# Optimization experiments

Measured on AMD Instinct MI355X. Metric: run time of the kernel, lower is better.

The kernel has to match this reference:

```python
import jax, jax.numpy as jnp
import numpy as np

EPS = 1e-5
TOPK = 2
SHARED_RATIO = 0.1

B, S, H = 2, 1024, 2048
NH, DH, R = 16, 128, 64
CQ, CKV = 1024, 512
E, I, NS = 8, 1024, 2


def rmsnorm(x, w):
    return x * jax.lax.rsqrt(jnp.mean(x * x, axis=-1, keepdims=True) + EPS) * w


def rope_cos_sin(seq_len, dim):
    inv = 1.0 / (10000.0 ** (jnp.arange(0, dim, 2, dtype=jnp.float32) / dim))
    t = jnp.arange(seq_len, dtype=jnp.float32)[:, None] * inv[None, :]  # [S, dim/2]
    return jnp.cos(t), jnp.sin(t)


def apply_rope(x, cos, sin):
    # rotate-half on last dim; cos/sin broadcast over leading dims
    x1, x2 = jnp.split(x, 2, axis=-1)
    return jnp.concatenate([x1 * cos - x2 * sin, x2 * cos + x1 * sin], axis=-1)


def swiglu(x, w1, w3, w2):
    return (jax.nn.silu(x @ w1) * (x @ w3)) @ w2


def setup_inputs() -> dict:
    key = jax.random.key(0)
    ks = jax.random.split(key, 24)
    sc = 0.02
    d = {
        'x': jax.random.normal(ks[0], (B, S, H), jnp.float32),
        'attn_norm_w': jnp.ones((H,), jnp.float32),
        'ffn_norm_w': jnp.ones((H,), jnp.float32),
        'W_dq': sc * jax.random.normal(ks[1], (H, CQ), jnp.float32),
        'q_norm_w': jnp.ones((CQ,), jnp.float32),
        'W_uq': sc * jax.random.normal(ks[2], (CQ, NH * DH), jnp.float32),
        'W_qr': sc * jax.random.normal(ks[3], (CQ, NH * R), jnp.float32),
        'W_dkv': sc * jax.random.normal(ks[4], (H, CKV), jnp.float32),
        'kv_norm_w': jnp.ones((CKV,), jnp.float32),
        'W_uk': sc * jax.random.normal(ks[5], (CKV, NH * DH), jnp.float32),
        'W_uv': sc * jax.random.normal(ks[6], (CKV, NH * DH), jnp.float32),
        'W_kr': sc * jax.random.normal(ks[7], (H, R), jnp.float32),
        'W_o': sc * jax.random.normal(ks[8], (NH * DH, H), jnp.float32),
        'centroids': sc * jax.random.normal(ks[9], (E, H), jnp.float32),
        'expert_bias': jnp.zeros((E,), jnp.float32),
        'w1': sc * jax.random.normal(ks[10], (E, H, I), jnp.float32),
        'w3': sc * jax.random.normal(ks[11], (E, H, I), jnp.float32),
        'w2': sc * jax.random.normal(ks[12], (E, I, H), jnp.float32),
        'w1s': sc * jax.random.normal(ks[13], (NS, H, I), jnp.float32),
        'w3s': sc * jax.random.normal(ks[14], (NS, H, I), jnp.float32),
        'w2s': sc * jax.random.normal(ks[15], (NS, I, H), jnp.float32),
    }
    return d


def reference(x, attn_norm_w, ffn_norm_w, W_dq, q_norm_w, W_uq, W_qr, W_dkv,
              kv_norm_w, W_uk, W_uv, W_kr, W_o, centroids, expert_bias,
              w1, w3, w2, w1s, w3s, w2s):
    b, s, h = x.shape
    r = W_kr.shape[1]
    nh = W_qr.shape[1] // r
    dh = W_uq.shape[1] // nh

    # ---- MLA attention (pre-norm) ----
    hn = rmsnorm(x, attn_norm_w)
    cq = rmsnorm(hn @ W_dq, q_norm_w)                    # [b,s,CQ] compressed query latent
    q = (cq @ W_uq).reshape(b, s, nh, dh)                # content queries
    qr = (cq @ W_qr).reshape(b, s, nh, r)                # rope queries
    ckv = rmsnorm(hn @ W_dkv, kv_norm_w)                 # [b,s,CKV] compressed kv latent
    k = (ckv @ W_uk).reshape(b, s, nh, dh)
    v = (ckv @ W_uv).reshape(b, s, nh, dh)
    kr = hn @ W_kr                                       # [b,s,r] shared rope key

    cos, sin = rope_cos_sin(s, r)
    qr = apply_rope(qr, cos[None, :, None, :], sin[None, :, None, :])
    kr = apply_rope(kr, cos[None, :, :], sin[None, :, :])

    scale = 1.0 / np.sqrt(dh + r).astype(np.float32)
    scores = (jnp.einsum('bqhd,bkhd->bhqk', q, k)
              + jnp.einsum('bqhr,bkr->bhqk', qr, kr)) * scale
    causal = jnp.tril(jnp.ones((s, s), dtype=bool))
    scores = jnp.where(causal[None, None], scores, jnp.finfo(scores.dtype).min)
    attn = jax.nn.softmax(scores, axis=-1)
    attn_out = jnp.einsum('bhqk,bkhd->bqhd', attn, v).reshape(b, s, nh * dh) @ W_o
    x = x + attn_out

    # ---- aux-loss-free MoE (pre-norm) ----
    h2 = rmsnorm(x, ffn_norm_w).reshape(b * s, h)
    gate_scores = jax.nn.sigmoid(h2 @ centroids.T)       # [T,E]
    _, idx = jax.lax.top_k(gate_scores + expert_bias[None, :], TOPK)  # bias only for selection
    gw = jnp.take_along_axis(gate_scores, idx, axis=1)
    gw = gw / jnp.sum(gw, axis=1, keepdims=True)
    dense_w = jnp.sum(jax.nn.one_hot(idx, gate_scores.shape[1], dtype=h2.dtype) * gw[..., None], axis=1)  # [T,E]

    moe = jnp.zeros_like(h2)
    for e in range(w1.shape[0]):
        moe = moe + dense_w[:, e:e + 1] * swiglu(h2, w1[e], w3[e], w2[e])
    for si in range(w1s.shape[0]):
        moe = moe + SHARED_RATIO * swiglu(h2, w1s[si], w3s[si], w2s[si])

    return x + moe.reshape(b, s, h)
```

## Files before the change

### kernel.cpp

```cpp
#include <hip/hip_runtime.h>
#include <hip/hip_bf16.h>
#include <math.h>

typedef unsigned short u16;
typedef __attribute__((ext_vector_type(8))) short s8v;
typedef __attribute__((ext_vector_type(4))) short s4v;
typedef __attribute__((ext_vector_type(4))) float f4v;

#define B_   2
#define S_   1024
#define T_   2048
#define H_   2048
#define NH_  16
#define DH_  128
#define R_   64
#define CQ_  1024
#define CKV_ 512
#define DQK_ 192
#define E_   8
#define I_   1024
#define NS_  2

__device__ __forceinline__ float us2f(u16 u){
  unsigned int i = ((unsigned int)u) << 16; float f; __builtin_memcpy(&f, &i, 4); return f;
}
__device__ __forceinline__ u16 f2us(float f){
  unsigned int i; __builtin_memcpy(&i, &f, 4);
  unsigned int r = i + 0x7fffu + ((i >> 16) & 1u);
  return (u16)(r >> 16);
}
__device__ __forceinline__ f4v MFMA_B16(s8v a, s8v b, f4v c){
  return __builtin_amdgcn_mfma_f32_16x16x32_bf16(a, b, c, 0, 0, 0);
}

typedef const __attribute__((address_space(1))) void* gas_ptr;
typedef __attribute__((address_space(3))) void* las_ptr;
__device__ __forceinline__ void gload16(const void* g, void* l){
  __builtin_amdgcn_global_load_lds((gas_ptr)g, (las_ptr)l, 16, 0, 0);
}

__global__ void rope_table_kernel(float* __restrict__ cosT, float* __restrict__ sinT){
  int i = blockIdx.x * 256 + threadIdx.x;
  if (i >= S_ * 32) return;
  int s = i >> 5, f = i & 31;
  double inv = exp(-(double)f / 32.0 * log(10000.0));
  double t = (double)s * inv;
  cosT[i] = (float)cos(t);
  sinT[i] = (float)sin(t);
}

__global__ __launch_bounds__(256) void ttc_kernel(const float* __restrict__ in, u16* __restrict__ outp,
                                                  int Kd, int Nd, size_t zs, int rowoff){
  __shared__ float tile[64][65];
  size_t ibase = (size_t)blockIdx.z * Kd * Nd;
  size_t obase = (size_t)blockIdx.z * zs;
  int k0 = blockIdx.y * 64, n0 = blockIdx.x * 64;
  int tid = threadIdx.x;
  int tx = tid & 15, ty = tid >> 4;
  #pragma unroll
  for (int pp = 0; pp < 4; pp++){
    int kk = pp * 16 + ty;
    f4v v = *(const f4v*)(in + ibase + (size_t)(k0 + kk) * Nd + n0 + tx * 4);
    tile[kk][tx * 4 + 0] = v[0];
    tile[kk][tx * 4 + 1] = v[1];
    tile[kk][tx * 4 + 2] = v[2];
    tile[kk][tx * 4 + 3] = v[3];
  }
  __syncthreads();
  #pragma unroll
  for (int pp = 0; pp < 4; pp++){
    int nn = pp * 16 + ty;
    s4v o;
    #pragma unroll
    for (int j = 0; j < 4; j++) o[j] = (short)f2us(tile[tx * 4 + j][nn]);
    *(s4v*)(outp + obase + (size_t)(rowoff + n0 + nn) * Kd + k0 + tx * 4) = o;
  }
}

__global__ __launch_bounds__(256) void rmsnorm_kernel(const float* __restrict__ in, const float* __restrict__ w,
                                                      u16* __restrict__ outb, float* __restrict__ outf, int D){
  int t = blockIdx.x;
  const float* row = in + (size_t)t * D;
  float ss = 0.f;
  for (int i = threadIdx.x * 4; i < D; i += 1024){
    f4v v = *(const f4v*)(row + i);
    ss += v[0]*v[0] + v[1]*v[1] + v[2]*v[2] + v[3]*v[3];
  }
  #pragma unroll
  for (int m = 1; m < 64; m <<= 1) ss += __shfl_xor(ss, m);
  __shared__ float red[4];
  if ((threadIdx.x & 63) == 0) red[threadIdx.x >> 6] = ss;
  __syncthreads();
  float tot = red[0] + red[1] + red[2] + red[3];
  float r = 1.0f / sqrtf(tot / (float)D + 1e-5f);
  for (int i = threadIdx.x * 4; i < D; i += 1024){
    f4v v = *(const f4v*)(row + i);
    f4v wv = *(const f4v*)(w + i);
    s4v ob;
    f4v of;
    #pragma unroll
    for (int j = 0; j < 4; j++){ of[j] = v[j] * r * wv[j]; ob[j] = (short)f2us(of[j]); }
    *(s4v*)(outb + (size_t)t * D + i) = ob;
    if (outf) *(f4v*)(outf + (size_t)t * D + i) = of;
  }
}

template<int OUTMODE, bool AGATHER>
__device__ __forceinline__ void gemm_core(const u16* __restrict__ A, int lda,
                                          const u16* __restrict__ Bt, int K, int M,
                                          const int* __restrict__ arows,
                                          float* __restrict__ outf0, float* __restrict__ outf1,
                                          float* __restrict__ outf2,
                                          u16* __restrict__ outb0, u16* __restrict__ outb1,
                                          int ldc0, int ldc1, int split, int split2,
                                          const float* __restrict__ resid,
                                          int bm0, int bn0){
  __shared__ u16 As[2][128 * 32];
  __shared__ u16 Bs[2][128 * 32];
  int tid = threadIdx.x;
  int w = tid >> 6, lane = tid & 63;
  int wr = w >> 2, wc = w & 3;
  int g = lane >> 4, l16 = lane & 15;

  f4v acc[4][2];
  #pragma unroll
  for (int m = 0; m < 4; m++)
    #pragma unroll
    for (int n = 0; n < 2; n++) acc[m][n] = (f4v)0.0f;

  int c = tid;
  int row = c >> 2;
  int sc = (c & 3) ^ ((c >> 3) & 3);
  int grow = bm0 + row;
  int ar;
  if (AGATHER) ar = arows[(grow < M) ? grow : 0];
  else         ar = (grow < M) ? grow : 0;
  const u16* asrc = A + (size_t)ar * lda + sc * 8;
  const u16* bsrc = Bt + (size_t)(bn0 + row) * K + sc * 8;
  int dst = (w * 64) * 8;
  int apos = (g ^ ((l16 >> 1) & 3)) * 8;

  int nt = K >> 5;
  gload16(asrc, &As[0][dst]);
  gload16(bsrc, &Bs[0][dst]);

  int cur = 0;
  for (int t = 0; t < nt; ++t){
    if (t + 1 < nt){
      int kn = (t + 1) * 32;
      gload16(asrc + kn, &As[cur ^ 1][dst]);
      gload16(bsrc + kn, &Bs[cur ^ 1][dst]);
      asm volatile("s_waitcnt vmcnt(2)" ::: "memory");
    } else {
      asm volatile("s_waitcnt vmcnt(0)" ::: "memory");
    }
    __builtin_amdgcn_s_barrier();
    asm volatile("" ::: "memory");
    s8v af[4], bf[2];
    #pragma unroll
    for (int m = 0; m < 4; m++) af[m] = *(const s8v*)(&As[cur][(wr * 64 + m * 16 + l16) * 32 + apos]);
    #pragma unroll
    for (int n = 0; n < 2; n++) bf[n] = *(const s8v*)(&Bs[cur][(wc * 32 + n * 16 + l16) * 32 + apos]);
    __builtin_amdgcn_s_setprio(1);
    #pragma unroll
    for (int m = 0; m < 4; m++)
      #pragma unroll
      for (int n = 0; n < 2; n++)
        acc[m][n] = MFMA_B16(af[m], bf[n], acc[m][n]);
    __builtin_amdgcn_s_setprio(0);
    asm volatile("" ::: "memory");
    __builtin_amdgcn_s_barrier();
    cur ^= 1;
  }

  #pragma unroll
  for (int m = 0; m < 4; m++)
    #pragma unroll
    for (int n = 0; n < 2; n++){
      int ccol = bn0 + wc * 32 + n * 16 + l16;
      #pragma unroll
      for (int j = 0; j < 4; j++){
        int r = wr * 64 + m * 16 + g * 4 + j;
        int gr = bm0 + r;
        if (gr >= M) continue;
        float v = acc[m][n][j];
        if (OUTMODE == 0){
          outf0[(size_t)gr * ldc0 + ccol] = v;
        } else if (OUTMODE == 1){
          outb0[(size_t)gr * ldc0 + ccol] = f2us(v);
        } else if (OUTMODE == 2){
          outf0[(size_t)gr * ldc0 + ccol] = v + resid[(size_t)gr * ldc0 + ccol];
        } else if (OUTMODE == 4){
          if (ccol < split) outb0[(size_t)gr * ldc0 + ccol] = f2us(v);
          else              outb1[(size_t)gr * ldc1 + (ccol - split)] = f2us(v);
        } else {
          if (ccol < split)       outf0[(size_t)gr * ldc0 + ccol] = v;
          else if (ccol < split2) outf1[(size_t)gr * ldc1 + (ccol - split)] = v;
          else if (ccol < split2 + 64) outf2[(size_t)gr * 64 + (ccol - split2)] = v;
        }
      }
    }
}

template<int OUTMODE>
__global__ __launch_bounds__(512) void gemm_kernel(const u16* __restrict__ A, int lda,
                                                   const u16* __restrict__ Bt, int K, int M,
                                                   float* __restrict__ outf0, float* __restrict__ outf1,
                                                   float* __restrict__ outf2,
                                                   u16* __restrict__ outb0, u16* __restrict__ outb1,
                                                   int ldc0, int ldc1, int split, int split2,
                                                   const float* __restrict__ resid){
  int gx = gridDim.x;
  int nwg = gx * gridDim.y;
  int orig = blockIdx.y * gx + blockIdx.x;
  int wg = orig;
  if ((nwg & 7) == 0) wg = (orig & 7) * (nwg >> 3) + (orig >> 3);
  int bx = wg % gx, by = wg / gx;
  gemm_core<OUTMODE, false>(A, lda, Bt, K, M, nullptr,
                            outf0, outf1, outf2, outb0, outb1, ldc0, ldc1, split, split2, resid,
                            by * 128, bx * 128);
}

__global__ __launch_bounds__(256) void build_qcat_kernel(const u16* __restrict__ qbuf, const u16* __restrict__ qrb,
                                                         const float* __restrict__ cosT, const float* __restrict__ sinT,
                                                         u16* __restrict__ qcat){
  size_t i8 = ((size_t)blockIdx.x * 256 + threadIdx.x) * 8;
  const size_t total = (size_t)B_ * NH_ * S_ * DQK_;
  if (i8 >= total) return;
  int d = (int)(i8 % DQK_); size_t rem = i8 / DQK_;
  int s = (int)(rem % S_); rem /= S_;
  int h = (int)(rem % NH_); int b = (int)(rem / NH_);
  int t = b * S_ + s;
  s8v o;
  if (d < DH_){
    o = *(const s8v*)(qbuf + (size_t)t * H_ + h * DH_ + d);
  } else {
    int r0 = d - DH_;
    int rr0 = r0 & 31;
    const u16* qp = qrb + (size_t)t * (NH_ * R_) + h * R_;
    #pragma unroll
    for (int j = 0; j < 8; j++){
      float c = cosT[s * 32 + rr0 + j], sn = sinT[s * 32 + rr0 + j];
      float lo = us2f(qp[rr0 + j]), hi = us2f(qp[rr0 + 32 + j]);
      float val = (r0 < 32) ? (lo * c - hi * sn) : (hi * c + lo * sn);
      o[j] = (short)f2us(val);
    }
  }
  *(s8v*)(qcat + i8) = o;
}

__global__ __launch_bounds__(256) void build_kcat_kernel(const u16* __restrict__ kbuf, const float* __restrict__ krb,
                                                         const float* __restrict__ cosT, const float* __restrict__ sinT,
                                                         u16* __restrict__ kcat){
  size_t i8 = ((size_t)blockIdx.x * 256 + threadIdx.x) * 8;
  const size_t total = (size_t)B_ * NH_ * S_ * DQK_;
  if (i8 >= total) return;
  int d = (int)(i8 % DQK_); size_t rem = i8 / DQK_;
  int s = (int)(rem % S_); rem /= S_;
  int h = (int)(rem % NH_); int b = (int)(rem / NH_);
  int t = b * S_ + s;
  s8v o;
  if (d < DH_){
    o = *(const s8v*)(kbuf + (size_t)t * H_ + h * DH_ + d);
  } else {
    int r0 = d - DH_;
    int rr0 = r0 & 31;
    const float* kp = krb + (size_t)t * R_;
    #pragma unroll
    for (int j = 0; j < 8; j++){
      float c = cosT[s * 32 + rr0 + j], sn = sinT[s * 32 + rr0 + j];
      float lo = kp[rr0 + j], hi = kp[rr0 + 32 + j];
      float val = (r0 < 32) ? (lo * c - hi * sn) : (hi * c + lo * sn);
      o[j] = (short)f2us(val);
    }
  }
  *(s8v*)(kcat + i8) = o;
}

__global__ __launch_bounds__(256) void build_vT_kernel(const u16* __restrict__ vbuf, u16* __restrict__ vT){
  __shared__ u16 tile[32][33];
  int bh = blockIdx.z; int b = bh >> 4, h = bh & 15;
  int s0 = blockIdx.x * 32, d0 = blockIdx.y * 32;
  int tx = threadIdx.x & 31, ty = threadIdx.x >> 5;
  for (int i = ty; i < 32; i += 8)
    tile[i][tx] = vbuf[(size_t)(b * S_ + s0 + i) * H_ + h * DH_ + d0 + tx];
  __syncthreads();
  for (int i = ty; i < 32; i += 8)
    vT[((size_t)bh * DH_ + d0 + i) * S_ + s0 + tx] = tile[tx][i];
}

__global__ __launch_bounds__(256) void attn_kernel(const u16* __restrict__ qcat, const u16* __restrict__ kcat,
                                                   const u16* __restrict__ vT, u16* __restrict__ aout){
  __shared__ u16 Ks[64 * 192];
  __shared__ u16 Vs[128 * 64];
  __shared__ u16 Ps[4][16][72];

  int qb = (int)(gridDim.x - 1) - (int)blockIdx.x;
  int h = blockIdx.y, b = blockIdx.z;
  int bh = b * NH_ + h;
  int tid = threadIdx.x;
  int w = tid >> 6, lane = tid & 63;
  int g = lane >> 4, l16 = lane & 15;
  int qrow0 = qb * 64 + w * 16;
// ... 107 lines not shown
    }
    __syncthreads();
  }

  float inv = 1.0f / lrow;
  int trow = b * S_ + qglob;
  #pragma unroll
  for (int dt = 0; dt < 8; dt++){
    s4v wv;
    #pragma unroll
    for (int j = 0; j < 4; j++) wv[j] = (short)f2us(o[dt][j] * inv);
    *(s4v*)(aout + (size_t)trow * H_ + h * DH_ + dt * 16 + g * 4) = wv;
  }
}

__global__ __launch_bounds__(64) void route_kernel(const float* __restrict__ h2f, const float* __restrict__ cent,
                                                   const float* __restrict__ bias,
                                                   int* __restrict__ eidx, float* __restrict__ ew,
                                                   int* __restrict__ counts){
  int t = blockIdx.x, lane = threadIdx.x;
  float acc[E_];
  #pragma unroll
  for (int e = 0; e < E_; e++) acc[e] = 0.f;
  for (int k = lane; k < H_; k += 64){
    float xv = h2f[(size_t)t * H_ + k];
    #pragma unroll
    for (int e = 0; e < E_; e++) acc[e] += xv * cent[(size_t)e * H_ + k];
  }
  #pragma unroll
  for (int m = 1; m < 64; m <<= 1)
    #pragma unroll
    for (int e = 0; e < E_; e++) acc[e] += __shfl_xor(acc[e], m);
  float s[E_], sb[E_];
  #pragma unroll
  for (int e = 0; e < E_; e++){ s[e] = 1.f / (1.f + expf(-acc[e])); sb[e] = s[e] + bias[e]; }
  int i0 = 0;
  #pragma unroll
  for (int e = 1; e < E_; e++) if (sb[e] > sb[i0]) i0 = e;
  int i1 = -1;
  #pragma unroll
  for (int e = 0; e < E_; e++) if (e != i0 && (i1 < 0 || sb[e] > sb[i1])) i1 = e;
  float w0 = s[i0], w1 = s[i1], nrm = w0 + w1;
  w0 /= nrm; w1 /= nrm;
  if (lane == 0){
    eidx[t * 2] = i0; eidx[t * 2 + 1] = i1;
    ew[t * 2] = w0; ew[t * 2 + 1] = w1;
    atomicAdd(&counts[i0], 1); atomicAdd(&counts[i1], 1);
  }
}

__global__ void scan_kernel(int* __restrict__ meta){
  if (threadIdx.x == 0 && blockIdx.x == 0){
    int off = 0;
    for (int e = 0; e < E_; e++){ meta[16 + e] = off; meta[32 + e] = meta[e]; off += meta[e]; }
    meta[16 + 8] = 4096; meta[32 + 8] = T_;
    meta[16 + 9] = 4096 + T_; meta[32 + 9] = T_;
  }
}

__global__ void fill_kernel(const int* __restrict__ eidx, const float* __restrict__ ew,
                            int* __restrict__ meta, int* __restrict__ rowlist, float* __restrict__ roww,
                            int* __restrict__ slotidx){
  int t = blockIdx.x * 256 + threadIdx.x;
  if (t >= T_) return;
  for (int j = 0; j < 2; j++){
    int e = eidx[t * 2 + j];
    int p = atomicAdd(&meta[8 + e], 1);
    int slot = meta[16 + e] + p;
    rowlist[slot] = t; roww[slot] = ew[t * 2 + j];
    slotidx[t * 2 + j] = slot;
  }
}

__global__ void init_shared_kernel(int* __restrict__ rowlist, float* __restrict__ roww){
  int i = blockIdx.x * 256 + threadIdx.x;
  if (i >= 2 * T_) return;
  rowlist[4096 + i] = i & (T_ - 1);
  roww[4096 + i] = 0.1f;
}

__global__ __launch_bounds__(512) void moe_gemm13_kernel(const u16* __restrict__ h2b,
    const u16* __restrict__ w13T, const u16* __restrict__ w13sT,
    const int* __restrict__ rowlist, const int* __restrict__ listoff, const int* __restrict__ cnt2,
    u16* __restrict__ t1b, u16* __restrict__ t3b){
  int e = blockIdx.z;
  int cnt = cnt2[e];
  if ((int)(blockIdx.y * 128) >= cnt) return;
  const u16* Bt = (e < 8) ? w13T + (size_t)e * 2048 * H_ : w13sT + (size_t)(e - 8) * 2048 * H_;
  int loff = listoff[e];
  gemm_core<4, true>(h2b, H_, Bt, H_, cnt, rowlist + loff,
                     nullptr, nullptr, nullptr, t1b + (size_t)loff * I_, t3b + (size_t)loff * I_,
                     I_, I_, 1024, 0, nullptr,
                     blockIdx.y * 128, blockIdx.x * 128);
}

__global__ __launch_bounds__(512) void moe_gemm2_kernel(const u16* __restrict__ ub,
    const u16* __restrict__ w2T, const u16* __restrict__ w2sT,
    const int* __restrict__ listoff, const int* __restrict__ cnt2,
    u16* __restrict__ o2){
  int e = blockIdx.z;
  int cnt = cnt2[e];
  if ((int)(blockIdx.y * 128) >= cnt) return;
  const u16* Bt = (e < 8) ? w2T + (size_t)e * H_ * I_ : w2sT + (size_t)(e - 8) * H_ * I_;
  int loff = listoff[e];
  gemm_core<1, false>(ub + (size_t)loff * I_, I_, Bt, I_, cnt, nullptr,
                      nullptr, nullptr, nullptr, o2 + (size_t)loff * H_, nullptr,
                      H_, 0, 0, 0, nullptr,
                      blockIdx.y * 128, blockIdx.x * 128);
}

__global__ __launch_bounds__(256) void silumul_kernel(const u16* __restrict__ t1b, const u16* __restrict__ t3b,
                                                      const float* __restrict__ roww, u16* __restrict__ ub){
  size_t i = ((size_t)blockIdx.x * 256 + threadIdx.x) * 8;
  if (i >= (size_t)8192 * I_) return;
  int row = (int)(i / I_);
  float w = roww[row];
  s8v a = *(const s8v*)(t1b + i);
  s8v b = *(const s8v*)(t3b + i);
  s8v o;
  #pragma unroll
  for (int j = 0; j < 8; j++){
    float av = us2f((u16)a[j]);
    float gm = av / (1.f + __expf(-av));
    o[j] = (short)f2us(gm * us2f((u16)b[j]) * w);
  }
  *(s8v*)(ub + i) = o;
}

__global__ __launch_bounds__(256) void combine_kernel(const float* __restrict__ x1, const u16* __restrict__ o2,
                                                      const int* __restrict__ slotidx, float* __restrict__ out){
  int t = blockIdx.x;
  int s0 = slotidx[2 * t], s1 = slotidx[2 * t + 1];
  const u16* r0 = o2 + (size_t)s0 * H_;
  const u16* r1 = o2 + (size_t)s1 * H_;
  const u16* r2 = o2 + (size_t)(4096 + t) * H_;
  const u16* r3 = o2 + (size_t)(4096 + T_ + t) * H_;
  const float* rx = x1 + (size_t)t * H_;
  float* ro = out + (size_t)t * H_;
  int c = threadIdx.x * 8;
  s8v v0 = *(const s8v*)(r0 + c);
  s8v v1 = *(const s8v*)(r1 + c);
  s8v v2 = *(const s8v*)(r2 + c);
  s8v v3 = *(const s8v*)(r3 + c);
  #pragma unroll
  for (int j = 0; j < 8; j++){
    ro[c + j] = rx[c + j] + us2f((u16)v0[j]) + us2f((u16)v1[j]) + us2f((u16)v2[j]) + us2f((u16)v3[j]);
  }
}

extern "C" void kernel_launch(void* const* d_in, const int* in_sizes, int n_in,
                              void* d_out, int out_size, void* d_ws, size_t ws_size,
                              hipStream_t stream){
  const float* x    = (const float*)d_in[0];
  const float* anw  = (const float*)d_in[1];
  const float* fnw  = (const float*)d_in[2];
  const float* Wdq  = (const float*)d_in[3];
  const float* qnw  = (const float*)d_in[4];
  const float* Wuq  = (const float*)d_in[5];
  const float* Wqr  = (const float*)d_in[6];
  const float* Wdkv = (const float*)d_in[7];
  const float* kvnw = (const float*)d_in[8];
  const float* Wuk  = (const float*)d_in[9];
  const float* Wuv  = (const float*)d_in[10];
  const float* Wkr  = (const float*)d_in[11];
  const float* Wo   = (const float*)d_in[12];
  const float* cent = (const float*)d_in[13];
  const float* ebias= (const float*)d_in[14];
  const float* w1   = (const float*)d_in[15];
  const float* w3   = (const float*)d_in[16];
  const float* w2   = (const float*)d_in[17];
  const float* w1s  = (const float*)d_in[18];
  const float* w3s  = (const float*)d_in[19];
  const float* w2s  = (const float*)d_in[20];
  float* out = (float*)d_out;

  char* p = (char*)d_ws;
  auto alloc = [&](size_t bytes)->void*{
    void* r = (void*)p; p += (bytes + 255) & ~(size_t)255; return r;
  };

  float* cosT = (float*)alloc((size_t)S_ * 32 * 4);
  float* sinT = (float*)alloc((size_t)S_ * 32 * 4);
  u16* WdqkvT = (u16*)alloc((size_t)1664 * H_ * 2);
  u16* WuqrT  = (u16*)alloc((size_t)3072 * CQ_ * 2);
  u16* WukvT  = (u16*)alloc((size_t)4096 * CKV_ * 2);
  u16* WoT   = (u16*)alloc((size_t)H_ * H_ * 2);
  u16* w13T  = (u16*)alloc((size_t)E_ * 2048 * H_ * 2);
  u16* w2T   = (u16*)alloc((size_t)E_ * H_ * I_ * 2);
  u16* w13sT = (u16*)alloc((size_t)NS_ * 2048 * H_ * 2);
  u16* w2sT  = (u16*)alloc((size_t)NS_ * H_ * I_ * 2);
  float* x1  = (float*)alloc((size_t)T_ * H_ * 4);
  float* h2f = (float*)alloc((size_t)T_ * H_ * 4);
  u16* h2b   = (u16*)alloc((size_t)T_ * H_ * 2);
  int* meta  = (int*)alloc(64 * 4);
  int* eidx  = (int*)alloc((size_t)T_ * 2 * 4);
  float* ew  = (float*)alloc((size_t)T_ * 2 * 4);
  int* rowlist = (int*)alloc(8192 * 4);
  float* roww  = (float*)alloc(8192 * 4);
  int* slotidx = (int*)alloc((size_t)T_ * 2 * 4);

  char* mark = p;
  u16* hn    = (u16*)alloc((size_t)T_ * H_ * 2);
  float* tq  = (float*)alloc((size_t)T_ * CQ_ * 4);
  u16* cq    = (u16*)alloc((size_t)T_ * CQ_ * 2);
  u16* qbuf  = (u16*)alloc((size_t)T_ * H_ * 2);
  u16* qrb   = (u16*)alloc((size_t)T_ * NH_ * R_ * 2);
  float* tkv = (float*)alloc((size_t)T_ * CKV_ * 4);
  u16* ckv   = (u16*)alloc((size_t)T_ * CKV_ * 2);
  u16* kbuf  = (u16*)alloc((size_t)T_ * H_ * 2);
  u16* vbuf  = (u16*)alloc((size_t)T_ * H_ * 2);
  float* krb = (float*)alloc((size_t)T_ * R_ * 4);
  u16* qcat  = (u16*)alloc((size_t)B_ * NH_ * S_ * DQK_ * 2);
  u16* kcat  = (u16*)alloc((size_t)B_ * NH_ * S_ * DQK_ * 2);
  u16* vT    = (u16*)alloc((size_t)B_ * NH_ * DH_ * S_ * 2);
  u16* aout  = (u16*)alloc((size_t)T_ * H_ * 2);

  p = mark;
  u16* t1b = (u16*)alloc((size_t)8192 * I_ * 2);
  u16* t3b = (u16*)alloc((size_t)8192 * I_ * 2);
  u16* ub  = (u16*)alloc((size_t)8192 * I_ * 2);
  u16* o2  = (u16*)alloc((size_t)8192 * H_ * 2);

  dim3 b256(256), b64(64), b512(512);

  hipMemsetAsync(meta, 0, 64 * 4, stream);
  hipMemsetAsync(WdqkvT + (size_t)1600 * H_, 0, (size_t)64 * H_ * 2, stream);

  rope_table_kernel<<<dim3((S_ * 32 + 255) / 256), b256, 0, stream>>>(cosT, sinT);

  ttc_kernel<<<dim3(CQ_ / 64, H_ / 64, 1),  b256, 0, stream>>>(Wdq,  WdqkvT, H_,  CQ_, 0, 0);
  ttc_kernel<<<dim3(CKV_ / 64, H_ / 64, 1), b256, 0, stream>>>(Wdkv, WdqkvT, H_,  CKV_, 0, 1024);
  ttc_kernel<<<dim3(1, H_ / 64, 1),         b256, 0, stream>>>(Wkr,  WdqkvT, H_,  R_, 0, 1536);
  ttc_kernel<<<dim3(H_ / 64, CQ_ / 64, 1),  b256, 0, stream>>>(Wuq,  WuqrT,  CQ_, H_, 0, 0);
  ttc_kernel<<<dim3(1024 / 64, CQ_ / 64, 1), b256, 0, stream>>>(Wqr, WuqrT,  CQ_, 1024, 0, 2048);
  ttc_kernel<<<dim3(H_ / 64, CKV_ / 64, 1), b256, 0, stream>>>(Wuk,  WukvT,  CKV_, H_, 0, 0);
  ttc_kernel<<<dim3(H_ / 64, CKV_ / 64, 1), b256, 0, stream>>>(Wuv,  WukvT,  CKV_, H_, 0, 2048);
  ttc_kernel<<<dim3(H_ / 64, H_ / 64, 1),   b256, 0, stream>>>(Wo,   WoT,    H_,  H_, 0, 0);
  ttc_kernel<<<dim3(I_ / 64, H_ / 64, E_),  b256, 0, stream>>>(w1,  w13T, H_, I_, (size_t)2048 * H_, 0);
  ttc_kernel<<<dim3(I_ / 64, H_ / 64, E_),  b256, 0, stream>>>(w3,  w13T, H_, I_, (size_t)2048 * H_, 1024);
  ttc_kernel<<<dim3(H_ / 64, I_ / 64, E_),  b256, 0, stream>>>(w2,  w2T,  I_, H_, (size_t)H_ * I_, 0);
  ttc_kernel<<<dim3(I_ / 64, H_ / 64, NS_), b256, 0, stream>>>(w1s, w13sT, H_, I_, (size_t)2048 * H_, 0);
  ttc_kernel<<<dim3(I_ / 64, H_ / 64, NS_), b256, 0, stream>>>(w3s, w13sT, H_, I_, (size_t)2048 * H_, 1024);
  ttc_kernel<<<dim3(H_ / 64, I_ / 64, NS_), b256, 0, stream>>>(w2s, w2sT, I_, H_, (size_t)H_ * I_, 0);

  rmsnorm_kernel<<<T_, b256, 0, stream>>>(x, anw, hn, nullptr, H_);

  gemm_kernel<5><<<dim3(1664 / 128, T_ / 128), b512, 0, stream>>>(hn, H_, WdqkvT, H_, T_,
      tq, tkv, krb, nullptr, nullptr, CQ_, CKV_, 1024, 1536, nullptr);
  rmsnorm_kernel<<<T_, b256, 0, stream>>>(tq, qnw, cq, nullptr, CQ_);
  rmsnorm_kernel<<<T_, b256, 0, stream>>>(tkv, kvnw, ckv, nullptr, CKV_);
  gemm_kernel<4><<<dim3(3072 / 128, T_ / 128), b512, 0, stream>>>(cq, CQ_, WuqrT, CQ_, T_,
      nullptr, nullptr, nullptr, qbuf, qrb, H_, NH_ * R_, 2048, 0, nullptr);
  gemm_kernel<4><<<dim3(4096 / 128, T_ / 128), b512, 0, stream>>>(ckv, CKV_, WukvT, CKV_, T_,
      nullptr, nullptr, nullptr, kbuf, vbuf, H_, H_, 2048, 0, nullptr);

  size_t qct = (size_t)B_ * NH_ * S_ * DQK_;
  build_qcat_kernel<<<dim3((qct / 8 + 255) / 256), b256, 0, stream>>>(qbuf, qrb, cosT, sinT, qcat);
  build_kcat_kernel<<<dim3((qct / 8 + 255) / 256), b256, 0, stream>>>(kbuf, krb, cosT, sinT, kcat);
  build_vT_kernel<<<dim3(S_ / 32, DH_ / 32, B_ * NH_), b256, 0, stream>>>(vbuf, vT);

  attn_kernel<<<dim3(S_ / 64, NH_, B_), b256, 0, stream>>>(qcat, kcat, vT, aout);

  gemm_kernel<2><<<dim3(H_ / 128, T_ / 128), b512, 0, stream>>>(aout, H_, WoT, H_, T_,
      x1, nullptr, nullptr, nullptr, nullptr, H_, 0, 0, 0, x);

  rmsnorm_kernel<<<T_, b256, 0, stream>>>(x1, fnw, h2b, h2f, H_);
  route_kernel<<<T_, b64, 0, stream>>>(h2f, cent, ebias, eidx, ew, meta);
  scan_kernel<<<dim3(1), b64, 0, stream>>>(meta);
  fill_kernel<<<dim3((T_ + 255) / 256), b256, 0, stream>>>(eidx, ew, meta, rowlist, roww, slotidx);
  init_shared_kernel<<<dim3((2 * T_ + 255) / 256), b256, 0, stream>>>(rowlist, roww);

  moe_gemm13_kernel<<<dim3(2048 / 128, 16, 10), b512, 0, stream>>>(h2b, w13T, w13sT,
      rowlist, meta + 16, meta + 32, t1b, t3b);
  silumul_kernel<<<dim3((8192 * I_ / 8 + 255) / 256), b256, 0, stream>>>(t1b, t3b, roww, ub);
  moe_gemm2_kernel<<<dim3(H_ / 128, 16, 10), b512, 0, stream>>>(ub, w2T, w2sT,
      meta + 16, meta + 32, o2);

  combine_kernel<<<T_, b256, 0, stream>>>(x1, o2, slotidx, out);
}
```

Before: 633.2 us.

## Fuse SiLU-gate into MoE up-projection GEMM and widen GEMM N-tiles to 256

Interleaves the w1 and w3 rows in the transposed weight buffer so adjacent output columns hold the gate and up values. The MoE gate/up GEMM can then apply SiLU, the multiply and the routing weight in its epilogue using a lane shuffle, and write the gated bf16 activation directly. This removes the separate silumul kernel and the t1/t3 intermediate buffers and their memory traffic. Separately, GEMM tiles are widened to 256 columns for several projections, which raises per-block reuse but doubles accumulator registers and B-tile LDS and halves the block count.

```diff
diff --git a/kernel.cpp b/kernel.cpp
--- a/kernel.cpp
+++ b/kernel.cpp
@@ -50,7 +50,7 @@
 }
 
 __global__ __launch_bounds__(256) void ttc_kernel(const float* __restrict__ in, u16* __restrict__ outp,
-                                                  int Kd, int Nd, size_t zs, int rowoff){
+                                                  int Kd, int Nd, size_t zs, int rowoff, int rowmul){
   __shared__ float tile[64][65];
   size_t ibase = (size_t)blockIdx.z * Kd * Nd;
   size_t obase = (size_t)blockIdx.z * zs;
@@ -73,7 +73,7 @@
     s4v o;
     #pragma unroll
     for (int j = 0; j < 4; j++) o[j] = (short)f2us(tile[tx * 4 + j][nn]);
-    *(s4v*)(outp + obase + (size_t)(rowoff + n0 + nn) * Kd + k0 + tx * 4) = o;
+    *(s4v*)(outp + obase + (size_t)(rowoff + (n0 + nn) * rowmul) * Kd + k0 + tx * 4) = o;
   }
 }
 
@@ -105,7 +105,7 @@
   }
 }
 
-template<int OUTMODE, bool AGATHER>
+template<int BN, int OUTMODE, bool AGATHER>
 __device__ __forceinline__ void gemm_core(const u16* __restrict__ A, int lda,
                                           const u16* __restrict__ Bt, int K, int M,
                                           const int* __restrict__ arows,
@@ -115,57 +115,72 @@
                                           int ldc0, int ldc1, int split, int split2,
                                           const float* __restrict__ resid,
                                           int bm0, int bn0){
+  constexpr int BP = BN / 128;
+  constexpr int NF = BN / 64;
   __shared__ u16 As[2][128 * 32];
-  __shared__ u16 Bs[2][128 * 32];
+  __shared__ u16 Bs[2][BN * 32];
   int tid = threadIdx.x;
   int w = tid >> 6, lane = tid & 63;
   int wr = w >> 2, wc = w & 3;
   int g = lane >> 4, l16 = lane & 15;
 
-  f4v acc[4][2];
+  f4v acc[4][NF];
   #pragma unroll
   for (int m = 0; m < 4; m++)
     #pragma unroll
-    for (int n = 0; n < 2; n++) acc[m][n] = (f4v)0.0f;
-
-  int c = tid;
-  int row = c >> 2;
-  int sc = (c & 3) ^ ((c >> 3) & 3);
-  int grow = bm0 + row;
+    for (int n = 0; n < NF; n++) acc[m][n] = (f4v)0.0f;
+
+  int ca = tid;
+  int rowa = ca >> 2;
+  int sca = (ca & 3) ^ ((ca >> 3) & 3);
+  int growa = bm0 + rowa;
   int ar;
-  if (AGATHER) ar = arows[(grow < M) ? grow : 0];
-  else         ar = (grow < M) ? grow : 0;
-  const u16* asrc = A + (size_t)ar * lda + sc * 8;
-  const u16* bsrc = Bt + (size_t)(bn0 + row) * K + sc * 8;
-  int dst = (w * 64) * 8;
+  if (AGATHER) ar = arows[(growa < M) ? growa : 0];
+  else         ar = (growa < M) ? growa : 0;
+  const u16* asrc = A + (size_t)ar * lda + sca * 8;
+  int dsta = (w * 64) * 8;
+
+  const u16* bsrc[BP];
+  int dstb[BP];
+  #pragma unroll
+  for (int p = 0; p < BP; p++){
+    int c = tid + p * 512;
+    int row = c >> 2;
+    int sc = (c & 3) ^ ((c >> 3) & 3);
+    bsrc[p] = Bt + (size_t)(bn0 + row) * K + sc * 8;
+    dstb[p] = (p * 512 + w * 64) * 8;
+  }
   int apos = (g ^ ((l16 >> 1) & 3)) * 8;
 
   int nt = K >> 5;
-  gload16(asrc, &As[0][dst]);
-  gload16(bsrc, &Bs[0][dst]);
+  gload16(asrc, &As[0][dsta]);
+  #pragma unroll
+  for (int p = 0; p < BP; p++) gload16(bsrc[p], &Bs[0][dstb[p]]);
 
   int cur = 0;
   for (int t = 0; t < nt; ++t){
     if (t + 1 < nt){
       int kn = (t + 1) * 32;
-      gload16(asrc + kn, &As[cur ^ 1][dst]);
-      gload16(bsrc + kn, &Bs[cur ^ 1][dst]);
-      asm volatile("s_waitcnt vmcnt(2)" ::: "memory");
+      gload16(asrc + kn, &As[cur ^ 1][dsta]);
+      #pragma unroll
+      for (int p = 0; p < BP; p++) gload16(bsrc[p] + kn, &Bs[cur ^ 1][dstb[p]]);
+      if (BP == 2) asm volatile("s_waitcnt vmcnt(3)" ::: "memory");
+      else         asm volatile("s_waitcnt vmcnt(2)" ::: "memory");
     } else {
       asm volatile("s_waitcnt vmcnt(0)" ::: "memory");
     }
     __builtin_amdgcn_s_barrier();
     asm volatile("" ::: "memory");
-    s8v af[4], bf[2];
+    s8v af[4], bf[NF];
     #pragma unroll
     for (int m = 0; m < 4; m++) af[m] = *(const s8v*)(&As[cur][(wr * 64 + m * 16 + l16) * 32 + apos]);
     #pragma unroll
-    for (int n = 0; n < 2; n++) bf[n] = *(const s8v*)(&Bs[cur][(wc * 32 + n * 16 + l16) * 32 + apos]);
+    for (int n = 0; n < NF; n++) bf[n] = *(const s8v*)(&Bs[cur][(wc * (BN / 4) + n * 16 + l16) * 32 + apos]);
     __builtin_amdgcn_s_setprio(1);
     #pragma unroll
     for (int m = 0; m < 4; m++)
       #pragma unroll
-      for (int n = 0; n < 2; n++)
+      for (int n = 0; n < NF; n++)
         acc[m][n] = MFMA_B16(af[m], bf[n], acc[m][n]);
     __builtin_amdgcn_s_setprio(0);
     asm volatile("" ::: "memory");
@@ -176,14 +191,23 @@
   #pragma unroll
   for (int m = 0; m < 4; m++)
     #pragma unroll
-    for (int n = 0; n < 2; n++){
-      int ccol = bn0 + wc * 32 + n * 16 + l16;
+    for (int n = 0; n < NF; n++){
+      int ccol = bn0 + wc * (BN / 4) + n * 16 + l16;
       #pragma unroll
       for (int j = 0; j < 4; j++){
         int r = wr * 64 + m * 16 + g * 4 + j;
         int gr = bm0 + r;
+        float v = acc[m][n][j];
+        if (OUTMODE == 6){
+          float other = __shfl_xor(v, 1);
+          if (gr < M && (lane & 1) == 0){
+            float wgt = resid[gr];
+            float gm = v / (1.f + __expf(-v));
+            outb0[(size_t)gr * ldc0 + (ccol >> 1)] = f2us(gm * other * wgt);
+          }
+          continue;
+        }
         if (gr >= M) continue;
-        float v = acc[m][n][j];
         if (OUTMODE == 0){
           outf0[(size_t)gr * ldc0 + ccol] = v;
         } else if (OUTMODE == 1){
@@ -202,7 +226,7 @@
     }
 }
 
-template<int OUTMODE>
+template<int BN, int OUTMODE>
 __global__ __launch_bounds__(512) void gemm_kernel(const u16* __restrict__ A, int lda,
                                                    const u16* __restrict__ Bt, int K, int M,
                                                    float* __restrict__ outf0, float* __restrict__ outf1,
@@ -216,9 +240,9 @@
   int wg = orig;
   if ((nwg & 7) == 0) wg = (orig & 7) * (nwg >> 3) + (orig >> 3);
   int bx = wg % gx, by = wg / gx;
-  gemm_core<OUTMODE, false>(A, lda, Bt, K, M, nullptr,
-                            outf0, outf1, outf2, outb0, outb1, ldc0, ldc1, split, split2, resid,
-                            by * 128, bx * 128);
+  gemm_core<BN, OUTMODE, false>(A, lda, Bt, K, M, nullptr,
+                                outf0, outf1, outf2, outb0, outb1, ldc0, ldc1, split, split2, resid,
+                                by * 128, bx * BN);
 }
 
 __global__ __launch_bounds__(256) void build_qcat_kernel(const u16* __restrict__ qbuf, const u16* __restrict__ qrb,
@@ -492,16 +516,16 @@
 __global__ __launch_bounds__(512) void moe_gemm13_kernel(const u16* __restrict__ h2b,
     const u16* __restrict__ w13T, const u16* __restrict__ w13sT,
     const int* __restrict__ rowlist, const int* __restrict__ listoff, const int* __restrict__ cnt2,
-    u16* __restrict__ t1b, u16* __restrict__ t3b){
+    const float* __restrict__ roww, u16* __restrict__ ub){
   int e = blockIdx.z;
   int cnt = cnt2[e];
   if ((int)(blockIdx.y * 128) >= cnt) return;
   const u16* Bt = (e < 8) ? w13T + (size_t)e * 2048 * H_ : w13sT + (size_t)(e - 8) * 2048 * H_;
   int loff = listoff[e];
-  gemm_core<4, true>(h2b, H_, Bt, H_, cnt, rowlist + loff,
-                     nullptr, nullptr, nullptr, t1b + (size_t)loff * I_, t3b + (size_t)loff * I_,
-                     I_, I_, 1024, 0, nullptr,
-                     blockIdx.y * 128, blockIdx.x * 128);
+  gemm_core<256, 6, true>(h2b, H_, Bt, H_, cnt, rowlist + loff,
+                          nullptr, nullptr, nullptr, ub + (size_t)loff * I_, nullptr,
+                          I_, 0, 0, 0, roww + loff,
+                          blockIdx.y * 128, blockIdx.x * 256);
 }
 
 __global__ __launch_bounds__(512) void moe_gemm2_kernel(const u16* __restrict__ ub,
@@ -513,28 +537,10 @@
   if ((int)(blockIdx.y * 128) >= cnt) return;
   const u16* Bt = (e < 8) ? w2T + (size_t)e * H_ * I_ : w2sT + (size_t)(e - 8) * H_ * I_;
   int loff = listoff[e];
-  gemm_core<1, false>(ub + (size_t)loff * I_, I_, Bt, I_, cnt, nullptr,
-                      nullptr, nullptr, nullptr, o2 + (size_t)loff * H_, nullptr,
-                      H_, 0, 0, 0, nullptr,
-                      blockIdx.y * 128, blockIdx.x * 128);
-}
-
-__global__ __launch_bounds__(256) void silumul_kernel(const u16* __restrict__ t1b, const u16* __restrict__ t3b,
-                                                      const float* __restrict__ roww, u16* __restrict__ ub){
-  size_t i = ((size_t)blockIdx.x * 256 + threadIdx.x) * 8;
-  if (i >= (size_t)8192 * I_) return;
-  int row = (int)(i / I_);
-  float w = roww[row];
-  s8v a = *(const s8v*)(t1b + i);
-  s8v b = *(const s8v*)(t3b + i);
-  s8v o;
-  #pragma unroll
-  for (int j = 0; j < 8; j++){
-    float av = us2f((u16)a[j]);
-    float gm = av / (1.f + __expf(-av));
-    o[j] = (short)f2us(gm * us2f((u16)b[j]) * w);
-  }
-  *(s8v*)(ub + i) = o;
+  gemm_core<256, 1, false>(ub + (size_t)loff * I_, I_, Bt, I_, cnt, nullptr,
+                           nullptr, nullptr, nullptr, o2 + (size_t)loff * H_, nullptr,
+                           H_, 0, 0, 0, nullptr,
+                           blockIdx.y * 128, blockIdx.x * 256);
 }
 
 __global__ __launch_bounds__(256) void combine_kernel(const float* __restrict__ x1, const u16* __restrict__ o2,
@@ -626,8 +632,6 @@
   u16* aout  = (u16*)alloc((size_t)T_ * H_ * 2);
 
   p = mark;
-  u16* t1b = (u16*)alloc((size_t)8192 * I_ * 2);
-  u16* t3b = (u16*)alloc((size_t)8192 * I_ * 2);
   u16* ub  = (u16*)alloc((size_t)8192 * I_ * 2);
   u16* o2  = (u16*)alloc((size_t)8192 * H_ * 2);
 
@@ -638,30 +642,30 @@
 
   rope_table_kernel<<<dim3((S_ * 32 + 255) / 256), b256, 0, stream>>>(cosT, sinT);
 
-  ttc_kernel<<<dim3(CQ_ / 64, H_ / 64, 1),  b256, 0, stream>>>(Wdq,  WdqkvT, H_,  CQ_, 0, 0);
-  ttc_kernel<<<dim3(CKV_ / 64, H_ / 64, 1), b256, 0, stream>>>(Wdkv, WdqkvT, H_,  CKV_, 0, 1024);
-  ttc_kernel<<<dim3(1, H_ / 64, 1),         b256, 0, stream>>>(Wkr,  WdqkvT, H_,  R_, 0, 1536);
-  ttc_kernel<<<dim3(H_ / 64, CQ_ / 64, 1),  b256, 0, stream>>>(Wuq,  WuqrT,  CQ_, H_, 0, 0);
-  ttc_kernel<<<dim3(1024 / 64, CQ_ / 64, 1), b256, 0, stream>>>(Wqr, WuqrT,  CQ_, 1024, 0, 2048);
-  ttc_kernel<<<dim3(H_ / 64, CKV_ / 64, 1), b256, 0, stream>>>(Wuk,  WukvT,  CKV_, H_, 0, 0);
-  ttc_kernel<<<dim3(H_ / 64, CKV_ / 64, 1), b256, 0, stream>>>(Wuv,  WukvT,  CKV_, H_, 0, 2048);
-  ttc_kernel<<<dim3(H_ / 64, H_ / 64, 1),   b256, 0, stream>>>(Wo,   WoT,    H_,  H_, 0, 0);
-  ttc_kernel<<<dim3(I_ / 64, H_ / 64, E_),  b256, 0, stream>>>(w1,  w13T, H_, I_, (size_t)2048 * H_, 0);
-  ttc_kernel<<<dim3(I_ / 64, H_ / 64, E_),  b256, 0, stream>>>(w3,  w13T, H_, I_, (size_t)2048 * H_, 1024);
-  ttc_kernel<<<dim3(H_ / 64, I_ / 64, E_),  b256, 0, stream>>>(w2,  w2T,  I_, H_, (size_t)H_ * I_, 0);
-  ttc_kernel<<<dim3(I_ / 64, H_ / 64, NS_), b256, 0, stream>>>(w1s, w13sT, H_, I_, (size_t)2048 * H_, 0);
-  ttc_kernel<<<dim3(I_ / 64, H_ / 64, NS_), b256, 0, stream>>>(w3s, w13sT, H_, I_, (size_t)2048 * H_, 1024);
-  ttc_kernel<<<dim3(H_ / 64, I_ / 64, NS_), b256, 0, stream>>>(w2s, w2sT, I_, H_, (size_t)H_ * I_, 0);
+  ttc_kernel<<<dim3(CQ_ / 64, H_ / 64, 1),  b256, 0, stream>>>(Wdq,  WdqkvT, H_,  CQ_, 0, 0, 1);
+  ttc_kernel<<<dim3(CKV_ / 64, H_ / 64, 1), b256, 0, stream>>>(Wdkv, WdqkvT, H_,  CKV_, 0, 1024, 1);
+  ttc_kernel<<<dim3(1, H_ / 64, 1),         b256, 0, stream>>>(Wkr,  WdqkvT, H_,  R_, 0, 1536, 1);
+  ttc_kernel<<<dim3(H_ / 64, CQ_ / 64, 1),  b256, 0, stream>>>(Wuq,  WuqrT,  CQ_, H_, 0, 0, 1);
+  ttc_kernel<<<dim3(1024 / 64, CQ_ / 64, 1), b256, 0, stream>>>(Wqr, WuqrT,  CQ_, 1024, 0, 2048, 1);
+  ttc_kernel<<<dim3(H_ / 64, CKV_ / 64, 1), b256, 0, stream>>>(Wuk,  WukvT,  CKV_, H_, 0, 0, 1);
+  ttc_kernel<<<dim3(H_ / 64, CKV_ / 64, 1), b256, 0, stream>>>(Wuv,  WukvT,  CKV_, H_, 0, 2048, 1);
+  ttc_kernel<<<dim3(H_ / 64, H_ / 64, 1),   b256, 0, stream>>>(Wo,   WoT,    H_,  H_, 0, 0, 1);
+  ttc_kernel<<<dim3(I_ / 64, H_ / 64, E_),  b256, 0, stream>>>(w1,  w13T, H_, I_, (size_t)2048 * H_, 0, 2);
+  ttc_kernel<<<dim3(I_ / 64, H_ / 64, E_),  b256, 0, stream>>>(w3,  w13T, H_, I_, (size_t)2048 * H_, 1, 2);
+  ttc_kernel<<<dim3(H_ / 64, I_ / 64, E_),  b256, 0, stream>>>(w2,  w2T,  I_, H_, (size_t)H_ * I_, 0, 1);
+  ttc_kernel<<<dim3(I_ / 64, H_ / 64, NS_), b256, 0, stream>>>(w1s, w13sT, H_, I_, (size_t)2048 * H_, 0, 2);
+  ttc_kernel<<<dim3(I_ / 64, H_ / 64, NS_), b256, 0, stream>>>(w3s, w13sT, H_, I_, (size_t)2048 * H_, 1, 2);
+  ttc_kernel<<<dim3(H_ / 64, I_ / 64, NS_), b256, 0, stream>>>(w2s, w2sT, I_, H_, (size_t)H_ * I_, 0, 1);
 
   rmsnorm_kernel<<<T_, b256, 0, stream>>>(x, anw, hn, nullptr, H_);
 
-  gemm_kernel<5><<<dim3(1664 / 128, T_ / 128), b512, 0, stream>>>(hn, H_, WdqkvT, H_, T_,
+  gemm_kernel<128, 5><<<dim3(1664 / 128, T_ / 128), b512, 0, stream>>>(hn, H_, WdqkvT, H_, T_,
       tq, tkv, krb, nullptr, nullptr, CQ_, CKV_, 1024, 1536, nullptr);
   rmsnorm_kernel<<<T_, b256, 0, stream>>>(tq, qnw, cq, nullptr, CQ_);
   rmsnorm_kernel<<<T_, b256, 0, stream>>>(tkv, kvnw, ckv, nullptr, CKV_);
-  gemm_kernel<4><<<dim3(3072 / 128, T_ / 128), b512, 0, stream>>>(cq, CQ_, WuqrT, CQ_, T_,
+  gemm_kernel<256, 4><<<dim3(3072 / 256, T_ / 128), b512, 0, stream>>>(cq, CQ_, WuqrT, CQ_, T_,
       nullptr, nullptr, nullptr, qbuf, qrb, H_, NH_ * R_, 2048, 0, nullptr);
-  gemm_kernel<4><<<dim3(4096 / 128, T_ / 128), b512, 0, stream>>>(ckv, CKV_, WukvT, CKV_, T_,
+  gemm_kernel<256, 4><<<dim3(4096 / 256, T_ / 128), b512, 0, stream>>>(ckv, CKV_, WukvT, CKV_, T_,
       nullptr, nullptr, nullptr, kbuf, vbuf, H_, H_, 2048, 0, nullptr);
 
   size_t qct = (size_t)B_ * NH_ * S_ * DQK_;
@@ -671,7 +675,7 @@
 
   attn_kernel<<<dim3(S_ / 64, NH_, B_), b256, 0, stream>>>(qcat, kcat, vT, aout);
 
-  gemm_kernel<2><<<dim3(H_ / 128, T_ / 128), b512, 0, stream>>>(aout, H_, WoT, H_, T_,
+  gemm_kernel<256, 2><<<dim3(H_ / 256, T_ / 128), b512, 0, stream>>>(aout, H_, WoT, H_, T_,
       x1, nullptr, nullptr, nullptr, nullptr, H_, 0, 0, 0, x);
 
   rmsnorm_kernel<<<T_, b256, 0, stream>>>(x1, fnw, h2b, h2f, H_);
@@ -680,10 +684,9 @@
   fill_kernel<<<dim3((T_ + 255) / 256), b256, 0, stream>>>(eidx, ew, meta, rowlist, roww, slotidx);
   init_shared_kernel<<<dim3((2 * T_ + 255) / 256), b256, 0, stream>>>(rowlist, roww);
 
-  moe_gemm13_kernel<<<dim3(2048 / 128, 16, 10), b512, 0, stream>>>(h2b, w13T, w13sT,
-      rowlist, meta + 16, meta + 32, t1b, t3b);
-  silumul_kernel<<<dim3((8192 * I_ / 8 + 255) / 256), b256, 0, stream>>>(t1b, t3b, roww, ub);
-  moe_gemm2_kernel<<<dim3(H_ / 128, 16, 10), b512, 0, stream>>>(ub, w2T, w2sT,
+  moe_gemm13_kernel<<<dim3(2048 / 256, 16, 10), b512, 0, stream>>>(h2b, w13T, w13sT,
+      rowlist, meta + 16, meta + 32, roww, ub);
+  moe_gemm2_kernel<<<dim3(H_ / 256, 16, 10), b512, 0, stream>>>(ub, w2T, w2sT,
       meta + 16, meta + 32, o2);
 
   combine_kernel<<<T_, b256, 0, stream>>>(x1, o2, slotidx, out);
```

Result: slower. 701.3 us (+10.8%).

## Fuse SiLU-gating into MoE gate/up GEMM epilogue via interleaved w1/w3 columns

Applied to the files above, without the earlier changes.

Interleaves the w1 and w3 columns in the transposed weight layout (row multiplier 2) so that adjacent output columns of the fused gate/up GEMM hold the w1 and w3 results for the same index. A new epilogue mode pairs lanes with a shuffle and writes silu(a)*b*routing_weight straight to the bf16 intermediate. This removes the separate silumul kernel and the t1/t3 intermediate round trips through memory. In exchange, half the lanes idle during the store, the stores are narrower, and the intermediate is no longer rounded to bf16 before the activation.

```diff
diff --git a/kernel.cpp b/kernel.cpp
--- a/kernel.cpp
+++ b/kernel.cpp
@@ -50,7 +50,7 @@
 }
 
 __global__ __launch_bounds__(256) void ttc_kernel(const float* __restrict__ in, u16* __restrict__ outp,
-                                                  int Kd, int Nd, size_t zs, int rowoff){
+                                                  int Kd, int Nd, size_t zs, int rowoff, int rowmul){
   __shared__ float tile[64][65];
   size_t ibase = (size_t)blockIdx.z * Kd * Nd;
   size_t obase = (size_t)blockIdx.z * zs;
@@ -73,7 +73,7 @@
     s4v o;
     #pragma unroll
     for (int j = 0; j < 4; j++) o[j] = (short)f2us(tile[tx * 4 + j][nn]);
-    *(s4v*)(outp + obase + (size_t)(rowoff + n0 + nn) * Kd + k0 + tx * 4) = o;
+    *(s4v*)(outp + obase + (size_t)(rowoff + (n0 + nn) * rowmul) * Kd + k0 + tx * 4) = o;
   }
 }
 
@@ -182,8 +182,17 @@
       for (int j = 0; j < 4; j++){
         int r = wr * 64 + m * 16 + g * 4 + j;
         int gr = bm0 + r;
+        float v = acc[m][n][j];
+        if (OUTMODE == 6){
+          float other = __shfl_xor(v, 1);
+          if (gr < M && (lane & 1) == 0){
+            float wgt = resid[gr];
+            float gm = v / (1.f + __expf(-v));
+            outb0[(size_t)gr * ldc0 + (ccol >> 1)] = f2us(gm * other * wgt);
+          }
+          continue;
+        }
         if (gr >= M) continue;
-        float v = acc[m][n][j];
         if (OUTMODE == 0){
           outf0[(size_t)gr * ldc0 + ccol] = v;
         } else if (OUTMODE == 1){
@@ -492,15 +501,15 @@
 __global__ __launch_bounds__(512) void moe_gemm13_kernel(const u16* __restrict__ h2b,
     const u16* __restrict__ w13T, const u16* __restrict__ w13sT,
     const int* __restrict__ rowlist, const int* __restrict__ listoff, const int* __restrict__ cnt2,
-    u16* __restrict__ t1b, u16* __restrict__ t3b){
+    const float* __restrict__ roww, u16* __restrict__ ub){
   int e = blockIdx.z;
   int cnt = cnt2[e];
   if ((int)(blockIdx.y * 128) >= cnt) return;
   const u16* Bt = (e < 8) ? w13T + (size_t)e * 2048 * H_ : w13sT + (size_t)(e - 8) * 2048 * H_;
   int loff = listoff[e];
-  gemm_core<4, true>(h2b, H_, Bt, H_, cnt, rowlist + loff,
-                     nullptr, nullptr, nullptr, t1b + (size_t)loff * I_, t3b + (size_t)loff * I_,
-                     I_, I_, 1024, 0, nullptr,
+  gemm_core<6, true>(h2b, H_, Bt, H_, cnt, rowlist + loff,
+                     nullptr, nullptr, nullptr, ub + (size_t)loff * I_, nullptr,
+                     I_, 0, 0, 0, roww + loff,
                      blockIdx.y * 128, blockIdx.x * 128);
 }
 
@@ -517,24 +526,6 @@
                       nullptr, nullptr, nullptr, o2 + (size_t)loff * H_, nullptr,
                       H_, 0, 0, 0, nullptr,
                       blockIdx.y * 128, blockIdx.x * 128);
-}
-
-__global__ __launch_bounds__(256) void silumul_kernel(const u16* __restrict__ t1b, const u16* __restrict__ t3b,
-                                                      const float* __restrict__ roww, u16* __restrict__ ub){
-  size_t i = ((size_t)blockIdx.x * 256 + threadIdx.x) * 8;
-  if (i >= (size_t)8192 * I_) return;
-  int row = (int)(i / I_);
-  float w = roww[row];
-  s8v a = *(const s8v*)(t1b + i);
-  s8v b = *(const s8v*)(t3b + i);
-  s8v o;
-  #pragma unroll
-  for (int j = 0; j < 8; j++){
-    float av = us2f((u16)a[j]);
-    float gm = av / (1.f + __expf(-av));
-    o[j] = (short)f2us(gm * us2f((u16)b[j]) * w);
-  }
-  *(s8v*)(ub + i) = o;
 }
 
 __global__ __launch_bounds__(256) void combine_kernel(const float* __restrict__ x1, const u16* __restrict__ o2,
@@ -626,8 +617,6 @@
   u16* aout  = (u16*)alloc((size_t)T_ * H_ * 2);
 
   p = mark;
-  u16* t1b = (u16*)alloc((size_t)8192 * I_ * 2);
-  u16* t3b = (u16*)alloc((size_t)8192 * I_ * 2);
   u16* ub  = (u16*)alloc((size_t)8192 * I_ * 2);
   u16* o2  = (u16*)alloc((size_t)8192 * H_ * 2);
 
@@ -638,20 +627,20 @@
 
   rope_table_kernel<<<dim3((S_ * 32 + 255) / 256), b256, 0, stream>>>(cosT, sinT);
 
-  ttc_kernel<<<dim3(CQ_ / 64, H_ / 64, 1),  b256, 0, stream>>>(Wdq,  WdqkvT, H_,  CQ_, 0, 0);
-  ttc_kernel<<<dim3(CKV_ / 64, H_ / 64, 1), b256, 0, stream>>>(Wdkv, WdqkvT, H_,  CKV_, 0, 1024);
-  ttc_kernel<<<dim3(1, H_ / 64, 1),         b256, 0, stream>>>(Wkr,  WdqkvT, H_,  R_, 0, 1536);
-  ttc_kernel<<<dim3(H_ / 64, CQ_ / 64, 1),  b256, 0, stream>>>(Wuq,  WuqrT,  CQ_, H_, 0, 0);
-  ttc_kernel<<<dim3(1024 / 64, CQ_ / 64, 1), b256, 0, stream>>>(Wqr, WuqrT,  CQ_, 1024, 0, 2048);
-  ttc_kernel<<<dim3(H_ / 64, CKV_ / 64, 1), b256, 0, stream>>>(Wuk,  WukvT,  CKV_, H_, 0, 0);
-  ttc_kernel<<<dim3(H_ / 64, CKV_ / 64, 1), b256, 0, stream>>>(Wuv,  WukvT,  CKV_, H_, 0, 2048);
-  ttc_kernel<<<dim3(H_ / 64, H_ / 64, 1),   b256, 0, stream>>>(Wo,   WoT,    H_,  H_, 0, 0);
-  ttc_kernel<<<dim3(I_ / 64, H_ / 64, E_),  b256, 0, stream>>>(w1,  w13T, H_, I_, (size_t)2048 * H_, 0);
-  ttc_kernel<<<dim3(I_ / 64, H_ / 64, E_),  b256, 0, stream>>>(w3,  w13T, H_, I_, (size_t)2048 * H_, 1024);
-  ttc_kernel<<<dim3(H_ / 64, I_ / 64, E_),  b256, 0, stream>>>(w2,  w2T,  I_, H_, (size_t)H_ * I_, 0);
-  ttc_kernel<<<dim3(I_ / 64, H_ / 64, NS_), b256, 0, stream>>>(w1s, w13sT, H_, I_, (size_t)2048 * H_, 0);
-  ttc_kernel<<<dim3(I_ / 64, H_ / 64, NS_), b256, 0, stream>>>(w3s, w13sT, H_, I_, (size_t)2048 * H_, 1024);
-  ttc_kernel<<<dim3(H_ / 64, I_ / 64, NS_), b256, 0, stream>>>(w2s, w2sT, I_, H_, (size_t)H_ * I_, 0);
+  ttc_kernel<<<dim3(CQ_ / 64, H_ / 64, 1),  b256, 0, stream>>>(Wdq,  WdqkvT, H_,  CQ_, 0, 0, 1);
+  ttc_kernel<<<dim3(CKV_ / 64, H_ / 64, 1), b256, 0, stream>>>(Wdkv, WdqkvT, H_,  CKV_, 0, 1024, 1);
+  ttc_kernel<<<dim3(1, H_ / 64, 1),         b256, 0, stream>>>(Wkr,  WdqkvT, H_,  R_, 0, 1536, 1);
+  ttc_kernel<<<dim3(H_ / 64, CQ_ / 64, 1),  b256, 0, stream>>>(Wuq,  WuqrT,  CQ_, H_, 0, 0, 1);
+  ttc_kernel<<<dim3(1024 / 64, CQ_ / 64, 1), b256, 0, stream>>>(Wqr, WuqrT,  CQ_, 1024, 0, 2048, 1);
+  ttc_kernel<<<dim3(H_ / 64, CKV_ / 64, 1), b256, 0, stream>>>(Wuk,  WukvT,  CKV_, H_, 0, 0, 1);
+  ttc_kernel<<<dim3(H_ / 64, CKV_ / 64, 1), b256, 0, stream>>>(Wuv,  WukvT,  CKV_, H_, 0, 2048, 1);
+  ttc_kernel<<<dim3(H_ / 64, H_ / 64, 1),   b256, 0, stream>>>(Wo,   WoT,    H_,  H_, 0, 0, 1);
+  ttc_kernel<<<dim3(I_ / 64, H_ / 64, E_),  b256, 0, stream>>>(w1,  w13T, H_, I_, (size_t)2048 * H_, 0, 2);
+  ttc_kernel<<<dim3(I_ / 64, H_ / 64, E_),  b256, 0, stream>>>(w3,  w13T, H_, I_, (size_t)2048 * H_, 1, 2);
+  ttc_kernel<<<dim3(H_ / 64, I_ / 64, E_),  b256, 0, stream>>>(w2,  w2T,  I_, H_, (size_t)H_ * I_, 0, 1);
+  ttc_kernel<<<dim3(I_ / 64, H_ / 64, NS_), b256, 0, stream>>>(w1s, w13sT, H_, I_, (size_t)2048 * H_, 0, 2);
+  ttc_kernel<<<dim3(I_ / 64, H_ / 64, NS_), b256, 0, stream>>>(w3s, w13sT, H_, I_, (size_t)2048 * H_, 1, 2);
+  ttc_kernel<<<dim3(H_ / 64, I_ / 64, NS_), b256, 0, stream>>>(w2s, w2sT, I_, H_, (size_t)H_ * I_, 0, 1);
 
   rmsnorm_kernel<<<T_, b256, 0, stream>>>(x, anw, hn, nullptr, H_);
 
@@ -681,8 +670,7 @@
   init_shared_kernel<<<dim3((2 * T_ + 255) / 256), b256, 0, stream>>>(rowlist, roww);
 
   moe_gemm13_kernel<<<dim3(2048 / 128, 16, 10), b512, 0, stream>>>(h2b, w13T, w13sT,
-      rowlist, meta + 16, meta + 32, t1b, t3b);
-  silumul_kernel<<<dim3((8192 * I_ / 8 + 255) / 256), b256, 0, stream>>>(t1b, t3b, roww, ub);
+      rowlist, meta + 16, meta + 32, roww, ub);
   moe_gemm2_kernel<<<dim3(H_ / 128, 16, 10), b512, 0, stream>>>(ub, w2T, w2sT,
       meta + 16, meta + 32, o2);
 
```

Result: no change. 631.0 us (-0.4%).
